# Kernel tuning notes

Hardware: AMD Instinct MI355X
Metric: run time of the kernel (lower is better)

Reference implementation:

```python
import jax, jax.numpy as jnp
import numpy as np

D = 1024      # model_dimension
H = 16        # num_heads
HD = D // H   # head_dimension (shared K/V head dim)
B, S = 2, 2048


def setup_inputs() -> dict:
    key = jax.random.key(0)
    ks = jax.random.split(key, 11)
    s = 0.02
    return {
        "q": jax.random.normal(ks[0], (B, S, D), jnp.float32),
        "k": jax.random.normal(ks[1], (B, S, D), jnp.float32),
        "v": jax.random.normal(ks[2], (B, S, D), jnp.float32),
        "Wq": jax.random.normal(ks[3], (D, D), jnp.float32) * s,
        "bq": jnp.zeros((D,), jnp.float32),
        "Wk": jax.random.normal(ks[4], (D, HD), jnp.float32) * s,
        "bk": jnp.zeros((HD,), jnp.float32),
        "Wv": jax.random.normal(ks[5], (D, HD), jnp.float32) * s,
        "bv": jnp.zeros((HD,), jnp.float32),
        "Wo": jax.random.normal(ks[6], (D, D), jnp.float32) * s,
        "bo": jnp.zeros((D,), jnp.float32),
    }


def reference(q, k, v, Wq, bq, Wk, bk, Wv, bv, Wo, bo):
    Bsz, Sq, Dm = q.shape
    # Q projection + split into heads: (B, H, Sq, HD)
    qh = (q @ Wq + bq).reshape(Bsz, Sq, H, HD).transpose(0, 2, 1, 3)
    # Shared single K/V head: (B, Sk, HD)
    kh = k @ Wk + bk
    vh = v @ Wv + bv
    # Scores (B, H, Sq, Sk), scaled then clamped as in the original
    scores = jnp.einsum('bhqd,bkd->bhqk', qh, kh) / jnp.sqrt(jnp.float32(HD))
    scores = jnp.clip(scores, -1e6, 1e6)
    attn = jax.nn.softmax(scores, axis=-1)
    out = jnp.einsum('bhqk,bkd->bhqd', attn, vh)
    out = out.transpose(0, 2, 1, 3).reshape(Bsz, Sq, Dm)
    return out @ Wo + bo
```

## Files before the change

### kernel.cpp

```cpp
#include <hip/hip_runtime.h>
#include <cstdint>
#include <cstddef>

typedef unsigned short u16;
typedef uint32_t u32;
typedef __bf16 bf16x8 __attribute__((ext_vector_type(8)));
typedef float  f32x4  __attribute__((ext_vector_type(4)));
typedef u16    u16x4  __attribute__((ext_vector_type(4)));
typedef u32    u32x4  __attribute__((ext_vector_type(4)));

#define DEV static __device__ __forceinline__
#define MFMA16(a, b, c) __builtin_amdgcn_mfma_f32_16x16x32_bf16(a, b, c, 0, 0, 0)

DEV u16 f2bf(float x) {
  unsigned u = __float_as_uint(x);
  u += 0x7fffu + ((u >> 16) & 1u);
  return (u16)(u >> 16);
}

DEV u32 cvt_pk_bf16(float lo, float hi) {
  u32 r;
  asm("v_cvt_pk_bf16_f32 %0, %1, %2" : "=v"(r) : "v"(lo), "v"(hi));
  return r;
}

DEV void gload_lds16(const void* g, void* l) {
  __builtin_amdgcn_global_load_lds(
      (__attribute__((address_space(1))) void*)(void*)g,
      (__attribute__((address_space(3))) void*)l, 16, 0, 0);
}

__global__ void k_transpose4(const float* __restrict__ Wq, u16* __restrict__ WqT,
                             const float* __restrict__ Wo, u16* __restrict__ WoT,
                             const float* __restrict__ Wk, u16* __restrict__ WkT,
                             const float* __restrict__ Wv, u16* __restrict__ WvT) {
  __shared__ float tile[32][33];
  const int z = blockIdx.z;
  const int C = z < 2 ? 1024 : 64;
  constexpr int R = 1024;
  if (blockIdx.x * 32 >= C) return;
  const float* in = z == 0 ? Wq : z == 1 ? Wo : z == 2 ? Wk : Wv;
  u16* out = z == 0 ? WqT : z == 1 ? WoT : z == 2 ? WkT : WvT;
  int bx = blockIdx.x * 32, by = blockIdx.y * 32;
  int tx = threadIdx.x, ty = threadIdx.y;
#pragma unroll
  for (int j = 0; j < 4; ++j)
    tile[ty + j * 8][tx] = in[(size_t)(by + ty + j * 8) * C + bx + tx];
  __syncthreads();
#pragma unroll
  for (int j = 0; j < 4; ++j)
    out[(size_t)(bx + ty + j * 8) * R + by + tx] = f2bf(tile[tx][ty + j * 8]);
}

template <bool OUT_BF16, bool A_FP32>
__global__ __launch_bounds__(512) void k_gemm128(const void* __restrict__ Ap, const u16* __restrict__ Bt,
                                                 const float* __restrict__ bias, void* __restrict__ Cout,
                                                 int M, int N, int K, float scale) {
  __shared__ u16 As[2][128 * 32];
  __shared__ u16 Bs[2][128 * 32];
  const int tid = threadIdx.x, lane = tid & 63, wid = tid >> 6;
  const int s = blockIdx.x;
  const int xr = s & 7, t = s >> 3;
  const int bx = t & 7;
  const int by = (t >> 3) * 8 + xr;
  const int brow = by * 128, bcol = bx * 128;
  const int wr = (wid >> 2) * 64, wc = (wid & 3) * 32;

  const int e0 = wid * 512 + lane * 8;
  const u16* b0 = Bt + (size_t)(bcol + (e0 >> 5)) * K + (e0 & 31);
  const u16* a0bf = A_FP32 ? nullptr : (const u16*)Ap + (size_t)(brow + (e0 >> 5)) * K + (e0 & 31);
  const float* a0f = A_FP32 ? (const float*)Ap + (size_t)(brow + (tid >> 2)) * K + (tid & 3) * 8 : nullptr;

  f32x4 ra0, ra1;
  auto LOADA = [&](int k0) {
    ra0 = *(const f32x4*)(a0f + k0);
    ra1 = *(const f32x4*)(a0f + k0 + 4);
  };
  auto WRITEA = [&](int buf) {
    u32x4 w;
    w[0] = cvt_pk_bf16(ra0[0], ra0[1]);
    w[1] = cvt_pk_bf16(ra0[2], ra0[3]);
    w[2] = cvt_pk_bf16(ra1[0], ra1[1]);
    w[3] = cvt_pk_bf16(ra1[2], ra1[3]);
    *(u32x4*)&As[buf][tid * 8] = w;
  };

  f32x4 acc[4][2] = {};
  const int NK = K / 32;
  if constexpr (A_FP32) {
    LOADA(0);
    gload_lds16(b0, &Bs[0][wid * 512]);
    WRITEA(0);
    LOADA(32);
    asm volatile("s_waitcnt lgkmcnt(0)" ::: "memory");
  } else {
    gload_lds16(a0bf, &As[0][wid * 512]);
    gload_lds16(b0, &Bs[0][wid * 512]);
  }
#pragma unroll 1
  for (int ks = 0; ks < NK; ++ks) {
    if (ks + 1 < NK) {
      if constexpr (A_FP32) {
        gload_lds16(b0 + (ks + 1) * 32, &Bs[(ks + 1) & 1][wid * 512]);
        asm volatile("s_waitcnt vmcnt(3)\n\ts_barrier" ::: "memory");
      } else {
        gload_lds16(a0bf + (ks + 1) * 32, &As[(ks + 1) & 1][wid * 512]);
        gload_lds16(b0 + (ks + 1) * 32, &Bs[(ks + 1) & 1][wid * 512]);
        asm volatile("s_waitcnt vmcnt(2)\n\ts_barrier" ::: "memory");
      }
    } else {
      asm volatile("s_waitcnt vmcnt(0)\n\ts_barrier" ::: "memory");
    }
    __builtin_amdgcn_sched_barrier(0);

    const u16* Ab = &As[ks & 1][0];
    const u16* Bb = &Bs[ks & 1][0];
    const int lr = lane & 15, lk = (lane >> 4) * 8;
    bf16x8 af[4], bfr[2];
#pragma unroll
    for (int m = 0; m < 4; ++m) af[m] = *(const bf16x8*)&Ab[(wr + m * 16 + lr) * 32 + lk];
#pragma unroll
    for (int n = 0; n < 2; ++n) bfr[n] = *(const bf16x8*)&Bb[(wc + n * 16 + lr) * 32 + lk];
    __builtin_amdgcn_s_setprio(1);
#pragma unroll
    for (int m = 0; m < 4; ++m)
#pragma unroll
      for (int n = 0; n < 2; ++n) acc[m][n] = MFMA16(af[m], bfr[n], acc[m][n]);
    __builtin_amdgcn_s_setprio(0);

    if constexpr (A_FP32) {
      if (ks + 1 < NK) {
        WRITEA((ks + 1) & 1);
        if (ks + 2 < NK) LOADA((ks + 2) * 32);
      }
      asm volatile("s_waitcnt lgkmcnt(0)\n\ts_barrier" ::: "memory");
    } else {
      asm volatile("s_barrier" ::: "memory");
    }
  }

  const int lr = lane & 15, lg = lane >> 4;
#pragma unroll
  for (int m = 0; m < 4; ++m)
#pragma unroll
    for (int n = 0; n < 2; ++n) {
      const int col = bcol + wc + n * 16 + lr;
      const float bv = bias ? bias[col] : 0.f;
#pragma unroll
      for (int r = 0; r < 4; ++r) {
        const int row = brow + wr + m * 16 + lg * 4 + r;
        float val = (acc[m][n][r] + bv) * scale;
        if constexpr (OUT_BF16) ((u16*)Cout)[(size_t)row * N + col] = f2bf(val);
        else ((float*)Cout)[(size_t)row * N + col] = val;
      }
    }
}

__global__ __launch_bounds__(256) void k_gemm64(const float* __restrict__ A0, const float* __restrict__ A1,
                                                const u16* __restrict__ Bt0, const u16* __restrict__ Bt1,
                                                const float* __restrict__ bias0, const float* __restrict__ bias1,
                                                u16* __restrict__ C0, u16* __restrict__ C1, int K) {
  __shared__ u16 As[2][64 * 32];
  __shared__ u16 Bs[2][64 * 32];
  const int sel = blockIdx.y;
  const float* Af = sel ? A1 : A0;
  const u16* Bt = sel ? Bt1 : Bt0;
  const float* bias = sel ? bias1 : bias0;
  const int tid = threadIdx.x, lane = tid & 63, wid = tid >> 6;
  const int brow = blockIdx.x * 64;
  const int e0 = wid * 512 + lane * 8;
  const u16* b0 = Bt + (size_t)(e0 >> 5) * K + (e0 & 31);
  const float* a0f = Af + (size_t)(brow + (tid >> 2)) * K + (tid & 3) * 8;

  f32x4 ra0, ra1;
  auto LOADA = [&](int k0) {
    ra0 = *(const f32x4*)(a0f + k0);
    ra1 = *(const f32x4*)(a0f + k0 + 4);
  };
  auto WRITEA = [&](int buf) {
    u32x4 w;
    w[0] = cvt_pk_bf16(ra0[0], ra0[1]);
    w[1] = cvt_pk_bf16(ra0[2], ra0[3]);
    w[2] = cvt_pk_bf16(ra1[0], ra1[1]);
    w[3] = cvt_pk_bf16(ra1[2], ra1[3]);
    *(u32x4*)&As[buf][tid * 8] = w;
  };

  f32x4 acc[4] = {};
  const int NK = K / 32;
  LOADA(0);
  gload_lds16(b0, &Bs[0][wid * 512]);
  WRITEA(0);
  LOADA(32);
  asm volatile("s_waitcnt lgkmcnt(0)" ::: "memory");
#pragma unroll 1
  for (int ks = 0; ks < NK; ++ks) {
    if (ks + 1 < NK) {
      gload_lds16(b0 + (ks + 1) * 32, &Bs[(ks + 1) & 1][wid * 512]);
      asm volatile("s_waitcnt vmcnt(3)\n\ts_barrier" ::: "memory");
    } else {
      asm volatile("s_waitcnt vmcnt(0)\n\ts_barrier" ::: "memory");
    }
    __builtin_amdgcn_sched_barrier(0);

    const u16* Ab = &As[ks & 1][0];
    const u16* Bb = &Bs[ks & 1][0];
    const int lr = lane & 15, lk = (lane >> 4) * 8;
    bf16x8 af = *(const bf16x8*)&Ab[(wid * 16 + lr) * 32 + lk];
    __builtin_amdgcn_s_setprio(1);
#pragma unroll
    for (int n = 0; n < 4; ++n) {
      bf16x8 bfr = *(const bf16x8*)&Bb[(n * 16 + lr) * 32 + lk];
      acc[n] = MFMA16(af, bfr, acc[n]);
    }
    __builtin_amdgcn_s_setprio(0);

    if (ks + 1 < NK) {
      WRITEA((ks + 1) & 1);
      if (ks + 2 < NK) LOADA((ks + 2) * 32);
    }
    asm volatile("s_waitcnt lgkmcnt(0)\n\ts_barrier" ::: "memory");
  }

  const int lr = lane & 15, lg = lane >> 4;
#pragma unroll
  for (int n = 0; n < 4; ++n) {
    const int col = n * 16 + lr;
    const float bv = bias[col];
#pragma unroll
    for (int r = 0; r < 4; ++r) {
      const int row = brow + wid * 16 + lg * 4 + r;
      const float val = acc[n][r] + bv;
      if (sel)
        C1[((size_t)(row >> 11) * 64 + col) * 2048 + (row & 2047)] = f2bf(val);
      else
        C0[(size_t)row * 64 + col] = f2bf(val);
    }
  }
}

__global__ __launch_bounds__(512) void k_attn(const float* __restrict__ qsrc, const u16* __restrict__ WqT,
                                              const float* __restrict__ bq,
                                              const u16* __restrict__ Kh, const u16* __restrict__ VhT,
                                              u16* __restrict__ Out) {
  constexpr int S = 2048, D = 1024, NT = 32, K = 1024;
  __shared__ __align__(16) char smem[49152];
  const int tid = threadIdx.x, lane = tid & 63, wid = tid >> 6;
  const int lr = lane & 15, lg = lane >> 4;
  const int q0 = blockIdx.x * 128;
  const int h = blockIdx.y;
  const int b = blockIdx.z;

  u16* AsQ = (u16*)smem;
  u16* BsQ = (u16*)(smem + 32768);
  u16* Qlds = (u16*)(smem + 32768);

  const int arow = tid >> 2, aq = tid & 3;
  const float* a0f = qsrc + (size_t)(b * S + q0 + arow) * K + aq * 16;
  const int bsrc_chunk = (tid & 7) ^ ((tid >> 3) & 7);
  const u16* b0q = WqT + (size_t)(h * 64 + (tid >> 3)) * K + bsrc_chunk * 8;

  f32x4 ra0, ra1, ra2, ra3;
  auto LOADA = [&](int k0) {
    ra0 = *(const f32x4*)(a0f + k0);
    ra1 = *(const f32x4*)(a0f + k0 + 4);
    ra2 = *(const f32x4*)(a0f + k0 + 8);
    ra3 = *(const f32x4*)(a0f + k0 + 12);
  };
  auto WRITEA = [&](int buf) {
    u32x4 w0, w1;
    w0[0] = cvt_pk_bf16(ra0[0], ra0[1]);
    w0[1] = cvt_pk_bf16(ra0[2], ra0[3]);
    w0[2] = cvt_pk_bf16(ra1[0], ra1[1]);
    w0[3] = cvt_pk_bf16(ra1[2], ra1[3]);
    w1[0] = cvt_pk_bf16(ra2[0], ra2[1]);
    w1[1] = cvt_pk_bf16(ra2[2], ra2[3]);
    w1[2] = cvt_pk_bf16(ra3[0], ra3[1]);
    w1[3] = cvt_pk_bf16(ra3[2], ra3[3]);
    char* base = (char*)AsQ + buf * 16384 + arow * 128;
    *(u32x4*)(base + (((aq * 2 + 0) ^ (arow & 7)) << 4)) = w0;
    *(u32x4*)(base + (((aq * 2 + 1) ^ (arow & 7)) << 4)) = w1;
  };

  {
    f32x4 accq[4] = {};
    LOADA(0);
    gload_lds16(b0q, BsQ + wid * 512);
    WRITEA(0);
    LOADA(64);
    asm volatile("s_waitcnt lgkmcnt(0)" ::: "memory");
#pragma unroll 1
    for (int ks = 0; ks < 16; ++ks) {
      if (ks + 1 < 16) {
        gload_lds16(b0q + (ks + 1) * 64, BsQ + ((ks + 1) & 1) * 4096 + wid * 512);
        asm volatile("s_waitcnt vmcnt(5)\n\ts_barrier" ::: "memory");
      } else {
        asm volatile("s_waitcnt vmcnt(0)\n\ts_barrier" ::: "memory");
      }
      __builtin_amdgcn_sched_barrier(0);

      const char* Ab = (const char*)AsQ + (ks & 1) * 16384;
      const char* Bb = (const char*)BsQ + (ks & 1) * 8192;
      bf16x8 af[2], bfr;
#pragma unroll
      for (int kk = 0; kk < 2; ++kk) {
        const int row = wid * 16 + lr;
        af[kk] = *(const bf16x8*)(Ab + row * 128 + (((kk * 4 + lg) ^ (row & 7)) << 4));
      }
      __builtin_amdgcn_s_setprio(1);
#pragma unroll
      for (int kk = 0; kk < 2; ++kk)
#pragma unroll
        for (int n = 0; n < 4; ++n) {
          const int row = n * 16 + lr;
          bfr = *(const bf16x8*)(Bb + row * 128 + (((kk * 4 + lg) ^ (row & 7)) << 4));
          accq[n] = MFMA16(af[kk], bfr, accq[n]);
        }
      __builtin_amdgcn_s_setprio(0);

      if (ks + 1 < 16) {
        WRITEA((ks + 1) & 1);
        if (ks + 2 < 16) LOADA((ks + 2) * 64);
      }
      asm volatile("s_waitcnt lgkmcnt(0)\n\ts_barrier" ::: "memory");
    }
    const float qscale = 0.125f * 1.44269504089f;
#pragma unroll
    for (int n = 0; n < 4; ++n) {
      const float bv = bq[h * 64 + n * 16 + lr];
#pragma unroll
      for (int r = 0; r < 4; ++r)
        Qlds[(wid * 16 + lg * 4 + r) * 64 + n * 16 + lr] = f2bf((accq[n][r] + bv) * qscale);
    }
    asm volatile("s_waitcnt lgkmcnt(0)\n\ts_barrier" ::: "memory");
  }

  u16* Ks0 = (u16*)smem;
  u16* Vs0 = (u16*)(smem + 16384);
  u16* Pw = Qlds + wid * (16 * 64);

  bf16x8 qf[2];
#pragma unroll
  for (int kk = 0; kk < 2; ++kk)
    qf[kk] = *(const bf16x8*)&Qlds[(wid * 16 + lr) * 64 + kk * 32 + lg * 8];

  const int r8 = lane >> 3, ssl = (lane & 7) ^ r8;
  const u16* ksrc = Kh + (size_t)(b * S + wid * 8 + r8) * 64 + ssl * 8;
  const u16* vsrc = VhT + (size_t)(b * 64 + wid * 8 + r8) * S + ssl * 8;

  float lsum = 0.f;
  f32x4 o[4] = {};
  const int pswz = (lr & 7) << 3;

  auto STAGE = [&](int buf, int t) {
    gload_lds16(ksrc + (size_t)(t * 64) * 64, &Ks0[buf * (64 * 64) + (wid * 8) * 64]);
    gload_lds16(vsrc + t * 64, &Vs0[buf * (64 * 64) + (wid * 8) * 64]);
  };

  STAGE(0, 0);
#pragma unroll 1
  for (int t = 0; t < NT; ++t) {
    if (t + 1 < NT) {
      STAGE((t + 1) & 1, t + 1);
      asm volatile("s_waitcnt vmcnt(2)\n\ts_barrier" ::: "memory");
    } else {
      asm volatile("s_waitcnt vmcnt(0)\n\ts_barrier" ::: "memory");
    }
    __builtin_amdgcn_sched_barrier(0);

    const u16* Kb = &Ks0[(t & 1) * (64 * 64)];
    const u16* Vb = &Vs0[(t & 1) * (64 * 64)];

    f32x4 z[4] = {};
    __builtin_amdgcn_s_setprio(1);
#pragma unroll
    for (int kk = 0; kk < 2; ++kk)
#pragma unroll
      for (int ct = 0; ct < 4; ++ct) {
        const int row = ct * 16 + lr;
        bf16x8 kf = *(const bf16x8*)&Kb[row * 64 + (((kk * 4 + lg) ^ (row & 7)) << 3)];
        z[ct] = MFMA16(kf, qf[kk], z[ct]);
      }
    __builtin_amdgcn_s_setprio(0);

    float s = 0.f;
#pragma unroll
    for (int ct = 0; ct < 4; ++ct) {
      const float p0 = __builtin_amdgcn_exp2f(z[ct][0]);
      const float p1 = __builtin_amdgcn_exp2f(z[ct][1]);
      const float p2 = __builtin_amdgcn_exp2f(z[ct][2]);
      const float p3 = __builtin_amdgcn_exp2f(z[ct][3]);
      s += (p0 + p1) + (p2 + p3);
      uint2 pk;
      pk.x = cvt_pk_bf16(p0, p1);
      pk.y = cvt_pk_bf16(p2, p3);
      *(uint2*)&Pw[lr * 64 + ((ct * 16 + lg * 4) ^ pswz)] = pk;
    }
    lsum += s;

#pragma unroll
    for (int kk = 0; kk < 2; ++kk) {
      bf16x8 pa = *(const bf16x8*)&Pw[lr * 64 + ((kk * 32 + lg * 8) ^ pswz)];
      __builtin_amdgcn_s_setprio(1);
#pragma unroll
      for (int nt = 0; nt < 4; ++nt) {
        const int row = nt * 16 + lr;
        bf16x8 vf = *(const bf16x8*)&Vb[row * 64 + (((kk * 4 + lg) ^ (row & 7)) << 3)];
        o[nt] = MFMA16(pa, vf, o[nt]);
      }
      __builtin_amdgcn_s_setprio(0);
    }
    asm volatile("s_barrier" ::: "memory");
  }

  lsum += __shfl_xor(lsum, 16);
  lsum += __shfl_xor(lsum, 32);
  const float linv = 1.f / lsum;
#pragma unroll
  for (int r = 0; r < 4; ++r) {
    const float li = __shfl(linv, (lane & 48) | (lg * 4 + r));
    const size_t row = (size_t)(b * S + q0 + wid * 16 + lg * 4 + r);
#pragma unroll
    for (int nt = 0; nt < 4; ++nt)
      Out[row * D + h * 64 + nt * 16 + lr] = f2bf(o[nt][r] * li);
  }
}

extern "C" void kernel_launch(void* const* d_in, const int* in_sizes, int n_in,
                              void* d_out, int out_size, void* d_ws, size_t ws_size,
                              hipStream_t stream) {
  const float* q  = (const float*)d_in[0];
  const float* k  = (const float*)d_in[1];
  const float* v  = (const float*)d_in[2];
  const float* Wq = (const float*)d_in[3];
  const float* bq = (const float*)d_in[4];
  const float* Wk = (const float*)d_in[5];
  const float* bk = (const float*)d_in[6];
  const float* Wv = (const float*)d_in[7];
  const float* bv = (const float*)d_in[8];
  const float* Wo = (const float*)d_in[9];
  const float* bo = (const float*)d_in[10];
  float* out = (float*)d_out;

  constexpr int B = 2, S = 2048, D = 1024, H = 16, HDc = 64;
  constexpr int M = B * S;

  char* ws = (char*)d_ws;
  size_t off = 0;
  auto alloc = [&](size_t bytes) { char* p = ws + off; off += bytes; return p; };
  u16* WqT  = (u16*)alloc((size_t)D * D * 2);
  u16* WkvT = (u16*)alloc((size_t)2 * HDc * D * 2);
  u16* WoT  = (u16*)alloc((size_t)D * D * 2);
  u16* Kh   = (u16*)alloc((size_t)M * HDc * 2);
  u16* VhT  = (u16*)alloc((size_t)M * HDc * 2);
  u16* AO   = (u16*)alloc((size_t)M * D * 2);
  u16* WkT = WkvT;
  u16* WvT = WkvT + (size_t)HDc * D;

  k_transpose4<<<dim3(32, 32, 4), dim3(32, 8), 0, stream>>>(Wq, WqT, Wo, WoT, Wk, WkT, Wv, WvT);
  k_gemm64<<<dim3(M / 64, 2), 256, 0, stream>>>(k, v, WkT, WvT, bk, bv, Kh, VhT, D);
  k_attn<<<dim3(S / 128, H, B), 512, 0, stream>>>(q, WqT, bq, Kh, VhT, AO);
  k_gemm128<false, false><<<dim3((M / 128) * (D / 128)), 512, 0, stream>>>(AO, WoT, bo, out, M, D, D, 1.0f);
}
```

Measured before the change: 110.6 us.

## Pre-convert q to bf16 in prep kernel and stage Q tiles via direct LDS loads

Adds a fifth z-slice to the weight-transpose kernel that converts the fp32 q input to a bf16 buffer. The fused attention kernel then loads Q-projection A tiles straight into LDS with global_load_lds instead of register loads, conversion and LDS stores. Each of the 16 head blocks per query tile used to re-read and re-convert the same fp32 q rows, so this halves that traffic and removes the per-head conversion work. The cost is an extra pass over q (read fp32, write bf16) and a new workspace buffer.

```diff
diff --git a/kernel.cpp b/kernel.cpp
--- a/kernel.cpp
+++ b/kernel.cpp
@@ -30,12 +30,28 @@
       (__attribute__((address_space(3))) void*)l, 16, 0, 0);
 }
 
-__global__ void k_transpose4(const float* __restrict__ Wq, u16* __restrict__ WqT,
-                             const float* __restrict__ Wo, u16* __restrict__ WoT,
-                             const float* __restrict__ Wk, u16* __restrict__ WkT,
-                             const float* __restrict__ Wv, u16* __restrict__ WvT) {
+__global__ void k_prep(const float* __restrict__ Wq, u16* __restrict__ WqT,
+                       const float* __restrict__ Wo, u16* __restrict__ WoT,
+                       const float* __restrict__ Wk, u16* __restrict__ WkT,
+                       const float* __restrict__ Wv, u16* __restrict__ WvT,
+                       const float* __restrict__ q, u16* __restrict__ qbf) {
   __shared__ float tile[32][33];
   const int z = blockIdx.z;
+  if (z == 4) {
+    const int bid = blockIdx.y * 32 + blockIdx.x;
+    const int tid = threadIdx.y * 32 + threadIdx.x;
+    const f32x4* src = (const f32x4*)q;
+    u16x4* dst = (u16x4*)qbf;
+#pragma unroll
+    for (int i = 0; i < 4; ++i) {
+      const int idx = bid * 1024 + i * 256 + tid;
+      f32x4 f = src[idx];
+      u16x4 o;
+      o[0] = f2bf(f[0]); o[1] = f2bf(f[1]); o[2] = f2bf(f[2]); o[3] = f2bf(f[3]);
+      dst[idx] = o;
+    }
+    return;
+  }
   const int C = z < 2 ? 1024 : 64;
   constexpr int R = 1024;
   if (blockIdx.x * 32 >= C) return;
@@ -239,7 +255,7 @@
   }
 }
 
-__global__ __launch_bounds__(512) void k_attn(const float* __restrict__ qsrc, const u16* __restrict__ WqT,
+__global__ __launch_bounds__(512) void k_attn(const u16* __restrict__ qbf, const u16* __restrict__ WqT,
                                               const float* __restrict__ bq,
                                               const u16* __restrict__ Kh, const u16* __restrict__ VhT,
                                               u16* __restrict__ Out) {
@@ -251,57 +267,37 @@
   const int h = blockIdx.y;
   const int b = blockIdx.z;
 
+  const int r8 = lane >> 3, ssl = (lane & 7) ^ r8;
+
   u16* AsQ = (u16*)smem;
   u16* BsQ = (u16*)(smem + 32768);
   u16* Qlds = (u16*)(smem + 32768);
 
-  const int arow = tid >> 2, aq = tid & 3;
-  const float* a0f = qsrc + (size_t)(b * S + q0 + arow) * K + aq * 16;
-  const int bsrc_chunk = (tid & 7) ^ ((tid >> 3) & 7);
-  const u16* b0q = WqT + (size_t)(h * 64 + (tid >> 3)) * K + bsrc_chunk * 8;
-
-  f32x4 ra0, ra1, ra2, ra3;
-  auto LOADA = [&](int k0) {
-    ra0 = *(const f32x4*)(a0f + k0);
-    ra1 = *(const f32x4*)(a0f + k0 + 4);
-    ra2 = *(const f32x4*)(a0f + k0 + 8);
-    ra3 = *(const f32x4*)(a0f + k0 + 12);
-  };
-  auto WRITEA = [&](int buf) {
-    u32x4 w0, w1;
-    w0[0] = cvt_pk_bf16(ra0[0], ra0[1]);
-    w0[1] = cvt_pk_bf16(ra0[2], ra0[3]);
-    w0[2] = cvt_pk_bf16(ra1[0], ra1[1]);
-    w0[3] = cvt_pk_bf16(ra1[2], ra1[3]);
-    w1[0] = cvt_pk_bf16(ra2[0], ra2[1]);
-    w1[1] = cvt_pk_bf16(ra2[2], ra2[3]);
-    w1[2] = cvt_pk_bf16(ra3[0], ra3[1]);
-    w1[3] = cvt_pk_bf16(ra3[2], ra3[3]);
-    char* base = (char*)AsQ + buf * 16384 + arow * 128;
-    *(u32x4*)(base + (((aq * 2 + 0) ^ (arow & 7)) << 4)) = w0;
-    *(u32x4*)(base + (((aq * 2 + 1) ^ (arow & 7)) << 4)) = w1;
-  };
-
   {
+    const u16* qa = qbf + (size_t)(b * S + q0 + wid * 16 + r8) * K + ssl * 8;
+    const u16* qb = WqT + (size_t)(h * 64 + wid * 8 + r8) * K + ssl * 8;
+
+    auto STAGEQ = [&](int buf, int ks) {
+      gload_lds16(qa + ks * 64, &AsQ[buf * 8192 + (wid * 16) * 64]);
+      gload_lds16(qa + ks * 64 + (size_t)8 * K, &AsQ[buf * 8192 + (wid * 16 + 8) * 64]);
+      gload_lds16(qb + ks * 64, &BsQ[buf * 4096 + (wid * 8) * 64]);
+    };
+
     f32x4 accq[4] = {};
-    LOADA(0);
-    gload_lds16(b0q, BsQ + wid * 512);
-    WRITEA(0);
-    LOADA(64);
-    asm volatile("s_waitcnt lgkmcnt(0)" ::: "memory");
+    STAGEQ(0, 0);
 #pragma unroll 1
     for (int ks = 0; ks < 16; ++ks) {
       if (ks + 1 < 16) {
-        gload_lds16(b0q + (ks + 1) * 64, BsQ + ((ks + 1) & 1) * 4096 + wid * 512);
-        asm volatile("s_waitcnt vmcnt(5)\n\ts_barrier" ::: "memory");
+        STAGEQ((ks + 1) & 1, ks + 1);
+        asm volatile("s_waitcnt vmcnt(3)\n\ts_barrier" ::: "memory");
       } else {
         asm volatile("s_waitcnt vmcnt(0)\n\ts_barrier" ::: "memory");
       }
       __builtin_amdgcn_sched_barrier(0);
 
-      const char* Ab = (const char*)AsQ + (ks & 1) * 16384;
-      const char* Bb = (const char*)BsQ + (ks & 1) * 8192;
-      bf16x8 af[2], bfr;
+      const char* Ab = (const char*)(AsQ + (ks & 1) * 8192);
+      const char* Bb = (const char*)(BsQ + (ks & 1) * 4096);
+      bf16x8 af[2];
 #pragma unroll
       for (int kk = 0; kk < 2; ++kk) {
         const int row = wid * 16 + lr;
@@ -313,17 +309,13 @@
 #pragma unroll
         for (int n = 0; n < 4; ++n) {
           const int row = n * 16 + lr;
-          bfr = *(const bf16x8*)(Bb + row * 128 + (((kk * 4 + lg) ^ (row & 7)) << 4));
+          bf16x8 bfr = *(const bf16x8*)(Bb + row * 128 + (((kk * 4 + lg) ^ (row & 7)) << 4));
           accq[n] = MFMA16(af[kk], bfr, accq[n]);
         }
       __builtin_amdgcn_s_setprio(0);
-
-      if (ks + 1 < 16) {
-        WRITEA((ks + 1) & 1);
-        if (ks + 2 < 16) LOADA((ks + 2) * 64);
-      }
-      asm volatile("s_waitcnt lgkmcnt(0)\n\ts_barrier" ::: "memory");
-    }
+      asm volatile("s_barrier" ::: "memory");
+    }
+    asm volatile("s_waitcnt lgkmcnt(0)\n\ts_barrier" ::: "memory");
     const float qscale = 0.125f * 1.44269504089f;
 #pragma unroll
     for (int n = 0; n < 4; ++n) {
@@ -344,7 +336,6 @@
   for (int kk = 0; kk < 2; ++kk)
     qf[kk] = *(const bf16x8*)&Qlds[(wid * 16 + lr) * 64 + kk * 32 + lg * 8];
 
-  const int r8 = lane >> 3, ssl = (lane & 7) ^ r8;
   const u16* ksrc = Kh + (size_t)(b * S + wid * 8 + r8) * 64 + ssl * 8;
   const u16* vsrc = VhT + (size_t)(b * 64 + wid * 8 + r8) * S + ssl * 8;
 
@@ -454,11 +445,12 @@
   u16* Kh   = (u16*)alloc((size_t)M * HDc * 2);
   u16* VhT  = (u16*)alloc((size_t)M * HDc * 2);
   u16* AO   = (u16*)alloc((size_t)M * D * 2);
+  u16* q_bf = (u16*)alloc((size_t)M * D * 2);
   u16* WkT = WkvT;
   u16* WvT = WkvT + (size_t)HDc * D;
 
-  k_transpose4<<<dim3(32, 32, 4), dim3(32, 8), 0, stream>>>(Wq, WqT, Wo, WoT, Wk, WkT, Wv, WvT);
+  k_prep<<<dim3(32, 32, 5), dim3(32, 8), 0, stream>>>(Wq, WqT, Wo, WoT, Wk, WkT, Wv, WvT, q, q_bf);
   k_gemm64<<<dim3(M / 64, 2), 256, 0, stream>>>(k, v, WkT, WvT, bk, bv, Kh, VhT, D);
-  k_attn<<<dim3(S / 128, H, B), 512, 0, stream>>>(q, WqT, bq, Kh, VhT, AO);
+  k_attn<<<dim3(S / 128, H, B), 512, 0, stream>>>(q_bf, WqT, bq, Kh, VhT, AO);
   k_gemm128<false, false><<<dim3((M / 128) * (D / 128)), 512, 0, stream>>>(AO, WoT, bo, out, M, D, D, 1.0f);
 }
```

Result: no change. 111.2 us (+0.6%).
